# Kernel optimization log

Measured on AMD Instinct MI355X. Metric: run time of the kernel, lower is better.

The kernel has to match this reference:

```python
import jax, jax.numpy as jnp
import numpy as np

P = 1024
H = 256
W = 256


def setup_inputs() -> dict:
    key = jax.random.key(0)
    k1, k2, k3, k4, k5, k6 = jax.random.split(key, 6)
    # Means in pixel coordinates, inside the image
    means_2d = jax.random.uniform(k1, (P, 2), dtype=jnp.float32) * jnp.array([W, H], dtype=jnp.float32)
    # Symmetric positive-definite 2x2 covariances packed as (a, b, c) = (cxx, cxy, cyy)
    a = 5.0 + 20.0 * jax.random.uniform(k2, (P,), dtype=jnp.float32)
    c = 5.0 + 20.0 * jax.random.uniform(k3, (P,), dtype=jnp.float32)
    b = (jax.random.uniform(k4, (P,), dtype=jnp.float32) - 0.5) * jnp.sqrt(a * c)  # |b| < 0.5*sqrt(ac) => det > 0
    covs_2d = jnp.stack([a, b, c], axis=-1)
    depth_features = 0.1 + 10.0 * jax.random.uniform(k5, (P,), dtype=jnp.float32)
    color_features = jax.random.uniform(k6, (P, 3), dtype=jnp.float32)
    return {
        "means_2d": means_2d,
        "covs_2d": covs_2d,
        "depth_features": depth_features,
        "color_features": color_features,
        "height": H,
        "width": W,
    }


def reference(means_2d, covs_2d, depth_features, color_features, height, width):
    # Front-to-back ordering by depth (nearest Gaussian composited first)
    order = jnp.argsort(depth_features)
    means = means_2d[order]          # [P,2]
    covs = covs_2d[order]            # [P,3]
    colors = color_features[order]   # [P,3]

    a, b, c = covs[:, 0], covs[:, 1], covs[:, 2]
    det = a * c - b * b
    ia = c / det
    ib = -b / det
    ic = a / det

    xs = jnp.arange(width, dtype=means.dtype) + 0.5   # pixel centers
    ys = jnp.arange(height, dtype=means.dtype) + 0.5
    dx = xs[None, None, :] - means[:, 0][:, None, None]   # [P,1,W]
    dy = ys[None, :, None] - means[:, 1][:, None, None]   # [P,H,1]

    # Mahalanobis distance under inverse 2D covariance (conic)
    q = (ia[:, None, None] * dx * dx
         + 2.0 * ib[:, None, None] * dx * dy
         + ic[:, None, None] * dy * dy)                   # [P,H,W]

    alpha = jnp.minimum(0.99, jnp.exp(-0.5 * q))
    alpha = jnp.where(alpha < 1.0 / 255.0, 0.0, alpha)    # 3DGS skip threshold

    # Exclusive cumulative transmittance along the depth-sorted axis
    T = jnp.cumprod(1.0 - alpha, axis=0)                  # [P,H,W]
    T_excl = jnp.concatenate([jnp.ones_like(T[:1]), T[:-1]], axis=0)
    w = alpha * T_excl                                    # per-Gaussian per-pixel weight

    img = jnp.einsum('pc,phw->chw', colors, w)            # [3,H,W]
    return img
```

## Files before the change

kernel.cpp:

```cpp
#include <hip/hip_runtime.h>
#include <cfloat>


constexpr int P_GAUSS = 1024;
constexpr int IMG_H = 256;
constexpr int IMG_W = 256;
constexpr float Q_GATE = 11.2f;
constexpr float Q_CULL = 11.3f;

constexpr int RAW_COVS  = 0;
constexpr int RAW_DEPTH = 3072;
constexpr int RAW_COLS  = 4096;
constexpr int RAW_TOT   = 7168;

__global__ __launch_bounds__(512) void gs_fused(
    const float* __restrict__ means,
    const float* __restrict__ covs,
    const float* __restrict__ depth,
    const float* __restrict__ colors,
    float* __restrict__ out)
{
    __shared__ float rawbuf[RAW_TOT];
    __shared__ float g[P_GAUSS * 8];
    __shared__ float g2[P_GAUSS * 8];
    __shared__ float sdepth[P_GAUSS + 4];
    __shared__ int   cnt16[16];

    const int tid = threadIdx.x;
    const int wid = tid >> 6;
    const int lane = tid & 63;

    const float tx0 = (float)(blockIdx.x * 16) + 0.5f;
    const float tx1 = tx0 + 15.0f;
    const float ty0 = (float)(blockIdx.y * 16) + 0.5f;
    const float ty1 = ty0 + 15.0f;

    {
        float4* rv = reinterpret_cast<float4*>(rawbuf);
        const float4* cv = reinterpret_cast<const float4*>(covs);
        const float4* dv = reinterpret_cast<const float4*>(depth);
        const float4* lv = reinterpret_cast<const float4*>(colors);
        rv[RAW_COVS / 4 + tid] = cv[tid];
        rv[RAW_COLS / 4 + tid] = lv[tid];
        if (tid < 256) {
            rv[RAW_COVS / 4 + 512 + tid] = cv[512 + tid];
            rv[RAW_COLS / 4 + 512 + tid] = lv[512 + tid];
            rv[RAW_DEPTH / 4 + tid]      = dv[tid];
        }
    }

    float mx[2], my[2], ca[2], cc[2];
    unsigned long long msk[2];
    bool hit[2];
#pragma unroll
    for (int r = 0; r < 2; ++r) {
        const int p = r * 512 + tid;
        const float2 m2 = reinterpret_cast<const float2*>(means)[p];
        mx[r] = m2.x; my[r] = m2.y;
        ca[r] = covs[3 * p + 0];
        cc[r] = covs[3 * p + 2];
        const float rx = sqrtf(Q_CULL * ca[r]);
        const float ry = sqrtf(Q_CULL * cc[r]);
        hit[r] = (mx[r] + rx >= tx0) && (mx[r] - rx <= tx1) &&
                 (my[r] + ry >= ty0) && (my[r] - ry <= ty1);
        msk[r] = __ballot(hit[r]);
        if (lane == 0) cnt16[r * 8 + wid] = __popcll(msk[r]);
    }
    __syncthreads();

    int c16[16];
#pragma unroll
    for (int k = 0; k < 16; ++k) c16[k] = cnt16[k];
    int total = 0;
#pragma unroll
    for (int k = 0; k < 16; ++k) total += c16[k];

#pragma unroll
    for (int r = 0; r < 2; ++r) {
        if (hit[r]) {
            const int p = r * 512 + tid;
            const float cb  = rawbuf[RAW_COVS + 3 * p + 1];
            const float dp  = rawbuf[RAW_DEPTH + p];
            const float cr  = rawbuf[RAW_COLS + 3 * p + 0];
            const float cg  = rawbuf[RAW_COLS + 3 * p + 1];
            const float cbl = rawbuf[RAW_COLS + 3 * p + 2];
            const int key = r * 8 + wid;
            int base = 0;
            for (int k = 0; k < key; ++k) base += c16[k];
            const int slot = base + __popcll(msk[r] & ((1ull << lane) - 1ull));
            float4* rec = reinterpret_cast<float4*>(g + slot * 8);
            rec[0] = make_float4(mx[r], my[r], ca[r], cb);
            rec[1] = make_float4(cc[r], cr, cg, cbl);
            sdepth[slot] = dp;
        }
    }
    if (tid < 4) sdepth[total + tid] = FLT_MAX;
    __syncthreads();

    const int limit4 = (total + 3) >> 2;
    for (int s = tid; s < total; s += 512) {
        const float d = sdepth[s];
        int rank = 0;
        const float4* sd4 = reinterpret_cast<const float4*>(sdepth);
        for (int jj = 0; jj < limit4; ++jj) {
            const float4 d4 = sd4[jj];
            const int j = 4 * jj;
            rank += (d4.x < d || (d4.x == d && j + 0 < s)) ? 1 : 0;
            rank += (d4.y < d || (d4.y == d && j + 1 < s)) ? 1 : 0;
            rank += (d4.z < d || (d4.z == d && j + 2 < s)) ? 1 : 0;
            rank += (d4.w < d || (d4.w == d && j + 3 < s)) ? 1 : 0;
        }
        const float4 r0 = reinterpret_cast<const float4*>(g + s * 8)[0];
        const float4 r1 = reinterpret_cast<const float4*>(g + s * 8)[1];
        const float a = r0.z, b = r0.w, c = r1.x;
        const float inv = 1.0f / (a * c - b * b);
        float4* dst = reinterpret_cast<float4*>(g2 + rank * 8);
        dst[0] = make_float4(r0.x, r0.y, c * inv, -b * inv);
        dst[1] = make_float4(a * inv, r1.y, r1.z, r1.w);
    }
    __syncthreads();

    if (tid < 256) {
        const float px = tx0 + (float)(tid & 15);
        const float py = ty0 + (float)(tid >> 4);

        float T = 1.0f;
        float acr = 0.0f, acg = 0.0f, acb = 0.0f;

        const float4* gv = reinterpret_cast<const float4*>(g2);
        float4 A0, B0, A1, B1;
        if (total > 0) { A0 = gv[0]; B0 = gv[1]; }
        if (total > 1) { A1 = gv[2]; B1 = gv[3]; }
        for (int p = 0; p < total; ++p) {
            const float4 c0 = A0;
            const float4 c1 = B0;
            A0 = A1; B0 = B1;
            if (p + 2 < total) { A1 = gv[2 * p + 4]; B1 = gv[2 * p + 5]; }
            const float dx = px - c0.x;
            const float dy = py - c0.y;
            const float q = c0.z * dx * dx + 2.0f * c0.w * (dx * dy) + c1.x * dy * dy;
            float alpha = fminf(0.99f, __expf(-0.5f * q));
            alpha = (q < Q_GATE && alpha >= (1.0f / 255.0f)) ? alpha : 0.0f;
            const float w = alpha * T;
            acr += w * c1.y;
            acg += w * c1.z;
            acb += w * c1.w;
            T *= (1.0f - alpha);
        }

        const int pix = (blockIdx.y * 16 + (tid >> 4)) * IMG_W + (blockIdx.x * 16 + (tid & 15));
        out[0 * IMG_H * IMG_W + pix] = acr;
        out[1 * IMG_H * IMG_W + pix] = acg;
        out[2 * IMG_H * IMG_W + pix] = acb;
    }
}

extern "C" void kernel_launch(void* const* d_in, const int* in_sizes, int n_in,
                              void* d_out, int out_size, void* d_ws, size_t ws_size,
                              hipStream_t stream) {
    const float* means  = (const float*)d_in[0];
    const float* covs   = (const float*)d_in[1];
    const float* depth  = (const float*)d_in[2];
    const float* colors = (const float*)d_in[3];
    float* out = (float*)d_out;

    gs_fused<<<dim3(IMG_W / 16, IMG_H / 16), dim3(512), 0, stream>>>(
        means, covs, depth, colors, out);
}
```

Baseline: 13.74 us.

## Split per-pixel compositing across both thread halves and drop intermediate record buffer

```diff
diff --git a/kernel.cpp b/kernel.cpp
--- a/kernel.cpp
+++ b/kernel.cpp
@@ -21,7 +21,6 @@
     float* __restrict__ out)
 {
     __shared__ float rawbuf[RAW_TOT];
-    __shared__ float g[P_GAUSS * 8];
     __shared__ float g2[P_GAUSS * 8];
     __shared__ float sdepth[P_GAUSS + 4];
     __shared__ int   cnt16[16];
@@ -75,6 +74,9 @@
 #pragma unroll
     for (int k = 0; k < 16; ++k) total += c16[k];
 
+    float4 rec0[2], rec1[2];
+    float dpr[2];
+    int slot[2];
 #pragma unroll
     for (int r = 0; r < 2; ++r) {
         if (hit[r]) {
@@ -87,68 +89,82 @@
             const int key = r * 8 + wid;
             int base = 0;
             for (int k = 0; k < key; ++k) base += c16[k];
-            const int slot = base + __popcll(msk[r] & ((1ull << lane) - 1ull));
-            float4* rec = reinterpret_cast<float4*>(g + slot * 8);
-            rec[0] = make_float4(mx[r], my[r], ca[r], cb);
-            rec[1] = make_float4(cc[r], cr, cg, cbl);
-            sdepth[slot] = dp;
+            const int s = base + __popcll(msk[r] & ((1ull << lane) - 1ull));
+            const float inv = 1.0f / (ca[r] * cc[r] - cb * cb);
+            rec0[r] = make_float4(mx[r], my[r], cc[r] * inv, -cb * inv);
+            rec1[r] = make_float4(ca[r] * inv, cr, cg, cbl);
+            dpr[r] = dp;
+            slot[r] = s;
+            sdepth[s] = dp;
         }
     }
     if (tid < 4) sdepth[total + tid] = FLT_MAX;
     __syncthreads();
 
     const int limit4 = (total + 3) >> 2;
-    for (int s = tid; s < total; s += 512) {
-        const float d = sdepth[s];
-        int rank = 0;
-        const float4* sd4 = reinterpret_cast<const float4*>(sdepth);
-        for (int jj = 0; jj < limit4; ++jj) {
-            const float4 d4 = sd4[jj];
-            const int j = 4 * jj;
-            rank += (d4.x < d || (d4.x == d && j + 0 < s)) ? 1 : 0;
-            rank += (d4.y < d || (d4.y == d && j + 1 < s)) ? 1 : 0;
-            rank += (d4.z < d || (d4.z == d && j + 2 < s)) ? 1 : 0;
-            rank += (d4.w < d || (d4.w == d && j + 3 < s)) ? 1 : 0;
+#pragma unroll
+    for (int r = 0; r < 2; ++r) {
+        if (hit[r]) {
+            const float d = dpr[r];
+            const int s = slot[r];
+            int rank = 0;
+            const float4* sd4 = reinterpret_cast<const float4*>(sdepth);
+            for (int jj = 0; jj < limit4; ++jj) {
+                const float4 d4 = sd4[jj];
+                const int j = 4 * jj;
+                rank += (d4.x < d || (d4.x == d && j + 0 < s)) ? 1 : 0;
+                rank += (d4.y < d || (d4.y == d && j + 1 < s)) ? 1 : 0;
+                rank += (d4.z < d || (d4.z == d && j + 2 < s)) ? 1 : 0;
+                rank += (d4.w < d || (d4.w == d && j + 3 < s)) ? 1 : 0;
+            }
+            float4* dst = reinterpret_cast<float4*>(g2 + rank * 8);
+            dst[0] = rec0[r];
+            dst[1] = rec1[r];
         }
-        const float4 r0 = reinterpret_cast<const float4*>(g + s * 8)[0];
-        const float4 r1 = reinterpret_cast<const float4*>(g + s * 8)[1];
-        const float a = r0.z, b = r0.w, c = r1.x;
-        const float inv = 1.0f / (a * c - b * b);
-        float4* dst = reinterpret_cast<float4*>(g2 + rank * 8);
-        dst[0] = make_float4(r0.x, r0.y, c * inv, -b * inv);
-        dst[1] = make_float4(a * inv, r1.y, r1.z, r1.w);
     }
     __syncthreads();
 
+    const int h = (total + 1) >> 1;
+    float4* part = reinterpret_cast<float4*>(rawbuf);
+    const float4* gv = reinterpret_cast<const float4*>(g2);
+
+    const int pixid = tid & 255;
+    const float px = tx0 + (float)(pixid & 15);
+    const float py = ty0 + (float)(pixid >> 4);
+    const int lo = (tid < 256) ? 0 : h;
+    const int hi = (tid < 256) ? h : total;
+
+    float T = 1.0f;
+    float acr = 0.0f, acg = 0.0f, acb = 0.0f;
+
+    float4 A0, B0, A1, B1;
+    if (lo + 0 < hi) { A0 = gv[2 * lo + 0]; B0 = gv[2 * lo + 1]; }
+    if (lo + 1 < hi) { A1 = gv[2 * lo + 2]; B1 = gv[2 * lo + 3]; }
+    for (int p = lo; p < hi; ++p) {
+        const float4 c0 = A0;
+        const float4 c1 = B0;
+        A0 = A1; B0 = B1;
+        if (p + 2 < hi) { A1 = gv[2 * p + 4]; B1 = gv[2 * p + 5]; }
+        const float dx = px - c0.x;
+        const float dy = py - c0.y;
+        const float q = c0.z * dx * dx + 2.0f * c0.w * (dx * dy) + c1.x * dy * dy;
+        float alpha = fminf(0.99f, __expf(-0.5f * q));
+        alpha = (q < Q_GATE && alpha >= (1.0f / 255.0f)) ? alpha : 0.0f;
+        const float w = alpha * T;
+        acr += w * c1.y;
+        acg += w * c1.z;
+        acb += w * c1.w;
+        T *= (1.0f - alpha);
+    }
+    if (tid >= 256) part[pixid] = make_float4(acr, acg, acb, T);
+    __syncthreads();
+
     if (tid < 256) {
-        const float px = tx0 + (float)(tid & 15);
-        const float py = ty0 + (float)(tid >> 4);
-
-        float T = 1.0f;
-        float acr = 0.0f, acg = 0.0f, acb = 0.0f;
-
-        const float4* gv = reinterpret_cast<const float4*>(g2);
-        float4 A0, B0, A1, B1;
-        if (total > 0) { A0 = gv[0]; B0 = gv[1]; }
-        if (total > 1) { A1 = gv[2]; B1 = gv[3]; }
-        for (int p = 0; p < total; ++p) {
-            const float4 c0 = A0;
-            const float4 c1 = B0;
-            A0 = A1; B0 = B1;
-            if (p + 2 < total) { A1 = gv[2 * p + 4]; B1 = gv[2 * p + 5]; }
-            const float dx = px - c0.x;
-            const float dy = py - c0.y;
-            const float q = c0.z * dx * dx + 2.0f * c0.w * (dx * dy) + c1.x * dy * dy;
-            float alpha = fminf(0.99f, __expf(-0.5f * q));
-            alpha = (q < Q_GATE && alpha >= (1.0f / 255.0f)) ? alpha : 0.0f;
-            const float w = alpha * T;
-            acr += w * c1.y;
-            acg += w * c1.z;
-            acb += w * c1.w;
-            T *= (1.0f - alpha);
-        }
-
-        const int pix = (blockIdx.y * 16 + (tid >> 4)) * IMG_W + (blockIdx.x * 16 + (tid & 15));
+        const float4 pb = part[pixid];
+        acr += T * pb.x;
+        acg += T * pb.y;
+        acb += T * pb.z;
+        const int pix = (blockIdx.y * 16 + (pixid >> 4)) * IMG_W + (blockIdx.x * 16 + (pixid & 15));
         out[0 * IMG_H * IMG_W + pix] = acr;
         out[1 * IMG_H * IMG_W + pix] = acg;
         out[2 * IMG_H * IMG_W + pix] = acb;
```

After: 14.68 us. 6.9% more time.
